# Performance work log

Measured on AMD Instinct MI355X. Metric: run time of the kernel, lower is better.

## Reference

```python
import jax, jax.numpy as jnp
import numpy as np

N = 4096      # nodes / sequence length
E = 131072    # edges (avg degree 32)
DIN = 512     # input feature dim
D = 256       # hidden_dim == output_dim (d_model)
H = 2         # nhead
DFF = 2048    # TransformerEncoderLayer default dim_feedforward
EPS = 1e-5


def setup_inputs() -> dict:
    key = jax.random.key(0)
    ks = jax.random.split(key, 16)
    s = lambda k, shape, scale: jax.random.normal(k, shape, jnp.float32) * scale
    return {
        "x": jax.random.normal(ks[0], (N, DIN), jnp.float32),
        "edge_index": jax.random.randint(ks[1], (2, E), 0, N),
        "edge_weight": jax.random.uniform(ks[2], (E,), jnp.float32),
        "W_gcn": s(ks[3], (DIN, D), 1.0 / np.sqrt(DIN)),
        "b_gcn": jnp.zeros((D,), jnp.float32),
        "in_proj_w": s(ks[4], (3 * D, D), 1.0 / np.sqrt(D)),
        "in_proj_b": jnp.zeros((3 * D,), jnp.float32),
        "out_proj_w": s(ks[5], (D, D), 1.0 / np.sqrt(D)),
        "out_proj_b": jnp.zeros((D,), jnp.float32),
        "lin1_w": s(ks[6], (DFF, D), 1.0 / np.sqrt(D)),
        "lin1_b": jnp.zeros((DFF,), jnp.float32),
        "lin2_w": s(ks[7], (D, DFF), 1.0 / np.sqrt(DFF)),
        "lin2_b": jnp.zeros((D,), jnp.float32),
        "ln1_g": jnp.ones((D,), jnp.float32),
        "ln1_b": jnp.zeros((D,), jnp.float32),
        "ln2_g": jnp.ones((D,), jnp.float32),
        "ln2_b": jnp.zeros((D,), jnp.float32),
    }


def _layernorm(x, g, b):
    mu = jnp.mean(x, axis=-1, keepdims=True)
    var = jnp.mean(jnp.square(x - mu), axis=-1, keepdims=True)
    return (x - mu) * jax.lax.rsqrt(var + EPS) * g + b


def _gcn_conv(x, edge_index, edge_weight, W, b):
    # PyG GCNConv: linear transform, add self-loops (weight 1), symmetric
    # degree normalization, scatter-add aggregation at target nodes.
    loops = jnp.arange(N)
    src = jnp.concatenate([edge_index[0], loops])
    dst = jnp.concatenate([edge_index[1], loops])
    w = jnp.concatenate([edge_weight, jnp.ones((N,), edge_weight.dtype)])
    deg = jax.ops.segment_sum(w, dst, num_segments=N)
    dinv = jnp.where(deg > 0, jax.lax.rsqrt(deg), 0.0)
    norm = dinv[src] * w * dinv[dst]                        # [E+N]
    xw = x @ W                                              # [N, D]
    out = jax.ops.segment_sum(norm[:, None] * xw[src], dst, num_segments=N)
    return out + b


def _mha(x, in_w, in_b, out_w, out_b):
    dh = D // H
    qkv = x @ in_w.T + in_b                                 # [N, 3D]
    q, k, v = jnp.split(qkv, 3, axis=-1)
    q = q.reshape(N, H, dh)
    k = k.reshape(N, H, dh)
    v = v.reshape(N, H, dh)
    scores = jnp.einsum("qhd,khd->hqk", q, k) / np.sqrt(dh)  # [H, N, N]
    attn = jax.nn.softmax(scores, axis=-1)
    o = jnp.einsum("hqk,khd->qhd", attn, v).reshape(N, D)
    return o @ out_w.T + out_b


def reference(x, edge_index, edge_weight, W_gcn, b_gcn, in_proj_w, in_proj_b,
              out_proj_w, out_proj_b, lin1_w, lin1_b, lin2_w, lin2_b,
              ln1_g, ln1_b, ln2_g, ln2_b):
    h = jax.nn.relu(_gcn_conv(x, edge_index, edge_weight, W_gcn, b_gcn))
    # TransformerEncoderLayer, post-norm (norm_first=False), dropout=eval
    h = _layernorm(h + _mha(h, in_proj_w, in_proj_b, out_proj_w, out_proj_b),
                   ln1_g, ln1_b)
    ff = jax.nn.relu(h @ lin1_w.T + lin1_b) @ lin2_w.T + lin2_b
    return _layernorm(h + ff, ln2_g, ln2_b)
```

## Files before the change

kernel.cpp:

```cpp
#include <hip/hip_runtime.h>
#include <hip/hip_bf16.h>

#define N_NODES 4096
#define E_EDGES 131072
#define DIN_    512
#define DM_     256
#define DFF_    2048
#define EPS_    1e-5f
#define NSPLIT  8

typedef __attribute__((ext_vector_type(8))) short bf16x8;
typedef __attribute__((ext_vector_type(4))) float f32x4;

__device__ __forceinline__ short f2b(float f) {
    union { float f; unsigned u; } x; x.f = f;
    unsigned r = x.u + 0x7fff + ((x.u >> 16) & 1);
    return (short)(r >> 16);
}

__device__ __forceinline__ void gload16(const void* g, void* l) {
    __builtin_amdgcn_global_load_lds(
        (const __attribute__((address_space(1))) void*)g,
        (__attribute__((address_space(3))) void*)l, 16, 0, 0);
}

__global__ __launch_bounds__(256)
void castall_kernel(const float* __restrict__ x, short* __restrict__ xb,
                    const float* __restrict__ inw, short* __restrict__ inwb,
                    const float* __restrict__ ow, short* __restrict__ owb,
                    const float* __restrict__ l1w, short* __restrict__ l1wb,
                    const float* __restrict__ l2w, short* __restrict__ l2wb,
                    const float* __restrict__ Wg, short* __restrict__ WgT) {
    const int b = blockIdx.x;
    __shared__ float t[32][33];
    if (b >= 3328) {
        const int b2 = b - 3328;
        const int bk = (b2 & 15) * 32, bn = (b2 >> 4) * 32;
        const int tx = threadIdx.x & 31, ty = threadIdx.x >> 5;
        #pragma unroll
        for (int i = 0; i < 4; ++i) {
            int r = ty + i * 8;
            t[r][tx] = Wg[(size_t)(bk + r) * DM_ + bn + tx];
        }
        __syncthreads();
        #pragma unroll
        for (int i = 0; i < 4; ++i) {
            int r = ty + i * 8;
            WgT[(size_t)(bn + r) * DIN_ + bk + tx] = f2b(t[tx][r]);
        }
        return;
    }
    const float* s; short* d; int base;
    if (b < 2048)      { s = x;   d = xb;   base = b * 256; }
    else if (b < 2240) { s = inw; d = inwb; base = (b - 2048) * 256; }
    else if (b < 2304) { s = ow;  d = owb;  base = (b - 2240) * 256; }
    else if (b < 2816) { s = l1w; d = l1wb; base = (b - 2304) * 256; }
    else               { s = l2w; d = l2wb; base = (b - 2816) * 256; }
    const int i = base + threadIdx.x;
    float4 v = reinterpret_cast<const float4*>(s)[i];
    union { short s[4]; int2 v; } o;
    o.s[0] = f2b(v.x); o.s[1] = f2b(v.y); o.s[2] = f2b(v.z); o.s[3] = f2b(v.w);
    reinterpret_cast<int2*>(d)[i] = o.v;
}

template<bool BF16OUT, bool RELU, bool SPLITK>
__global__ __launch_bounds__(256)
void mgemm_kernel(const short* __restrict__ A, const short* __restrict__ B,
                  const float* __restrict__ bias,
                  float* __restrict__ Cf, short* __restrict__ Cb,
                  short* __restrict__ VTout,
                  int M, int N, int K, int lda, int ldb, int ldc, int kchunk)
{
    __shared__ __align__(16) short As[128 * 32];
    __shared__ __align__(16) short Bs[128 * 32];
    const int tid = threadIdx.x;
    const int lane = tid & 63, w = tid >> 6;
    const int c = lane & 15, g = lane >> 4;
    const int wm = (w >> 1) * 64, wn = (w & 1) * 64;
    const int bm = blockIdx.y * 128, bn = blockIdx.x * 128;
    int k0 = 0, kend = K;
    if (SPLITK) { k0 = blockIdx.z * kchunk; kend = min(K, k0 + kchunk); }

    const int wbase = (tid & ~63) * 16;
    int srow[2], soff[2];
    #pragma unroll
    for (int i = 0; i < 2; ++i) {
        int L = i * 256 + tid;
        srow[i] = L >> 2;
        soff[i] = ((L & 3) ^ ((srow[i] >> 1) & 3)) * 8;
    }

    f32x4 acc[4][4] = {};
    for (int kb = k0; kb < kend; kb += 32) {
        #pragma unroll
        for (int i = 0; i < 2; ++i) {
            gload16(A + (size_t)(bm + srow[i]) * lda + kb + soff[i],
                    (char*)As + i * 4096 + wbase);
            gload16(B + (size_t)(bn + srow[i]) * ldb + kb + soff[i],
                    (char*)Bs + i * 4096 + wbase);
        }
        asm volatile("s_waitcnt vmcnt(0)" ::: "memory");
        __syncthreads();
        bf16x8 af[4], bf[4];
        #pragma unroll
        for (int mf = 0; mf < 4; ++mf) {
            int r = wm + mf * 16 + c;
            int sw = (g ^ ((r >> 1) & 3)) * 16;
            af[mf] = *reinterpret_cast<const bf16x8*>((const char*)As + r * 64 + sw);
        }
        #pragma unroll
        for (int nf = 0; nf < 4; ++nf) {
            int r = wn + nf * 16 + c;
            int sw = (g ^ ((r >> 1) & 3)) * 16;
            bf[nf] = *reinterpret_cast<const bf16x8*>((const char*)Bs + r * 64 + sw);
        }
        #pragma unroll
        for (int mf = 0; mf < 4; ++mf)
            #pragma unroll
            for (int nf = 0; nf < 4; ++nf)
                acc[mf][nf] = __builtin_amdgcn_mfma_f32_16x16x32_bf16(
                    af[mf], bf[nf], acc[mf][nf], 0, 0, 0);
        __syncthreads();
    }
    #pragma unroll
    for (int mf = 0; mf < 4; ++mf) {
        const int row = bm + wm + mf * 16 + g * 4;
        #pragma unroll
        for (int nf = 0; nf < 4; ++nf) {
            const int col = bn + wn + nf * 16 + c;
            float bv = bias ? bias[col] : 0.f;
            #pragma unroll
            for (int v = 0; v < 4; ++v) {
                float val = acc[mf][nf][v];
                size_t o = (size_t)(row + v) * ldc + col;
                if (SPLITK) {
                    if (blockIdx.z == 0) val += bv;
                    atomicAdd(&Cf[o], val);
                } else {
                    val += bv;
                    if (RELU) val = fmaxf(val, 0.f);
                    if (BF16OUT) {
                        short bvs = f2b(val);
                        Cb[o] = bvs;
                        if (VTout && col >= 512)
                            VTout[(size_t)(col - 512) * N_NODES + row + v] = bvs;
                    } else {
                        Cf[o] = val;
                    }
                }
            }
        }
    }
}

__global__ __launch_bounds__(256)
void fattn_kernel(const short* __restrict__ qkv, const short* __restrict__ VT,
                  short* __restrict__ Opart, float* __restrict__ ml)
{
    const int bid = blockIdx.x;
    const int j = bid >> 3;
    const int pair = 2 * (bid & 7) + (j & 1);
    const int hd = pair >> 3, sp = pair & 7;
    const int qt = j >> 1;
    const int tid = threadIdx.x;
    const int w = tid >> 6, lane = tid & 63;
    const int c = lane & 15, g = lane >> 4;
    const int q0 = qt * 64 + w * 16;

    __shared__ __align__(16) char smem[32768];
    char* KldsB = smem;
    char* VldsB = smem + 16384;
    short* Pw = (short*)(smem + w * 2816);

    const char* qkvC = (const char*)qkv;
    const char* vtC  = (const char*)VT;
    const int wbase = (tid & ~63) * 16;

    const short* Q = qkv + (size_t)q0 * 768 + hd * 128;
    bf16x8 qf[4];
    #pragma unroll
    for (int ks = 0; ks < 4; ++ks)
        qf[ks] = *reinterpret_cast<const bf16x8*>(Q + (size_t)c * 768 + ks * 32 + g * 8);

    auto stageKV = [&](int kt) {
        const int key0 = kt * 64;
        #pragma unroll
        for (int i = 0; i < 4; ++i) {
            int Lr  = i * 4096 + tid * 16;
            int key = Lr >> 8;
            int lg  = (Lr & 255) ^ ((key & 7) << 4);
            const char* src = qkvC + ((size_t)(key0 + key) * 768 + 256 + hd * 128) * 2 + lg;
            gload16(src, KldsB + i * 4096 + wbase);
        }
        #pragma unroll
        for (int i = 0; i < 4; ++i) {
            int Lr = i * 4096 + tid * 16;
            int dh = Lr >> 7;
            int lg = (Lr & 127) ^ ((dh & 7) << 4);
            const char* src = vtC + (size_t)(hd * 128 + dh) * 8192 + key0 * 2 + lg;
            gload16(src, VldsB + i * 4096 + wbase);
        }
    };

    f32x4 O[8] = {};
    float m[4]  = {-1e30f, -1e30f, -1e30f, -1e30f};
    float lsum[4] = {};
    const float C = 0.12751744f;

    stageKV(sp * 8);
    asm volatile("s_waitcnt vmcnt(0)" ::: "memory");
    __syncthreads();

    for (int t = 0; t < 8; ++t) {
        f32x4 S[4] = {};
        #pragma unroll
        for (int nf = 0; nf < 4; ++nf) {
            const int key = nf * 16 + c;
            const char* kr = KldsB + key * 256;
            const int sw = (key & 7) << 4;
            #pragma unroll
            for (int ks = 0; ks < 4; ++ks) {
                bf16x8 kf = *reinterpret_cast<const bf16x8*>(kr + ((ks * 64 + g * 16) ^ sw));
                S[nf] = __builtin_amdgcn_mfma_f32_16x16x32_bf16(qf[ks], kf, S[nf], 0, 0, 0);
            }
        }
        __syncthreads();

        float z[4][4];
        float lmax[4];
        bool ok = true;
        #pragma unroll
        for (int v = 0; v < 4; ++v) {
            #pragma unroll
            for (int nf = 0; nf < 4; ++nf) z[nf][v] = S[nf][v] * C;
            lmax[v] = fmaxf(fmaxf(z[0][v], z[1][v]), fmaxf(z[2][v], z[3][v]));
            ok = ok && (lmax[v] <= m[v] + 8.f);
        }
        if (!__all(ok)) {
            float mx[4];
            #pragma unroll
            for (int v = 0; v < 4; ++v) mx[v] = lmax[v];
            #pragma unroll
            for (int off = 1; off <= 8; off <<= 1)
                #pragma unroll
                for (int v = 0; v < 4; ++v) mx[v] = fmaxf(mx[v], __shfl_xor(mx[v], off));
            #pragma unroll
            for (int v = 0; v < 4; ++v) {
                float mn = fmaxf(m[v], mx[v]);
                float scl = exp2f(m[v] - mn);
                m[v] = mn;
                lsum[v] *= scl;
                #pragma unroll
                for (int nf2 = 0; nf2 < 8; ++nf2) O[nf2][v] *= scl;
            }
        }
        #pragma unroll
        for (int nf = 0; nf < 4; ++nf)
            #pragma unroll
            for (int v = 0; v < 4; ++v) {
                float p = exp2f(z[nf][v] - m[v]);
                lsum[v] += p;
                union { float f; unsigned u; } pu; pu.f = p;
                Pw[(4 * g + v) * 88 + nf * 16 + c] = (short)(pu.u >> 16);
            }
        bf16x8 pa[2];
        #pragma unroll
        for (int ks = 0; ks < 2; ++ks)
            pa[ks] = *reinterpret_cast<const bf16x8*>(Pw + c * 88 + ks * 32 + g * 8);
        #pragma unroll
        for (int nf2 = 0; nf2 < 8; ++nf2) {
            const int dh = nf2 * 16 + c;
            const char* vr = VldsB + dh * 128;
            const int sw = (dh & 7) << 4;
            #pragma unroll
            for (int ks = 0; ks < 2; ++ks) {
                bf16x8 vf = *reinterpret_cast<const bf16x8*>(vr + ((ks * 64 + g * 16) ^ sw));
                O[nf2] = __builtin_amdgcn_mfma_f32_16x16x32_bf16(pa[ks], vf, O[nf2], 0, 0, 0);
            }
        }
        __syncthreads();
        if (t < 7) {
            stageKV(sp * 8 + t + 1);
            asm volatile("s_waitcnt vmcnt(0)" ::: "memory");
            __syncthreads();
        }
    }
    #pragma unroll
    for (int off = 1; off <= 8; off <<= 1)
        #pragma unroll
        for (int v = 0; v < 4; ++v) lsum[v] += __shfl_xor(lsum[v], off);
    const size_t pbase = ((size_t)hd * NSPLIT + sp) * N_NODES;
    #pragma unroll
    for (int v = 0; v < 4; ++v) {
        const int row = q0 + 4 * g + v;
        const size_t rowo = (pbase + row) * 128;
        #pragma unroll
        for (int nf2 = 0; nf2 < 8; ++nf2)
            Opart[rowo + nf2 * 16 + c] = f2b(O[nf2][v]);
        if (c == 0) {
            ml[(pbase + row) * 2 + 0] = m[v];
            ml[(pbase + row) * 2 + 1] = lsum[v];
        }
    }
}

__global__ __launch_bounds__(256)
void attn_combine_kernel(const short* __restrict__ Opart, const float* __restrict__ ml,
                         short* __restrict__ attnb)
{
    const int row = blockIdx.x;
    const int hd = threadIdx.x >> 7, d = threadIdx.x & 127;
    float ms[NSPLIT], ls[NSPLIT];
    float mmax = -1e30f;
    #pragma unroll
    for (int s = 0; s < NSPLIT; ++s) {
        const size_t p = ((size_t)hd * NSPLIT + s) * N_NODES + row;
        ms[s] = ml[p * 2 + 0];
        ls[s] = ml[p * 2 + 1];
        mmax = fmaxf(mmax, ms[s]);
    }
    float lt = 0.f, acc = 0.f;
    #pragma unroll
    for (int s = 0; s < NSPLIT; ++s) {
        const float wgt = exp2f(ms[s] - mmax);
        lt += wgt * ls[s];
        const size_t p = ((size_t)hd * NSPLIT + s) * N_NODES + row;
        union { short s; unsigned short u; } b; b.s = Opart[p * 128 + d];
        union { unsigned u; float f; } cv; cv.u = ((unsigned)b.u) << 16;
        acc += wgt * cv.f;
    }
    attnb[(size_t)row * DM_ + hd * 128 + d] = f2b(acc / lt);
}

__global__ void deg_accum_kernel(const int* __restrict__ dst,
                                 const float* __restrict__ w,
                                 float* deg, int* count) {
    int e = blockIdx.x * 256 + threadIdx.x;
    if (e < E_EDGES) {
        int d = dst[e];
        atomicAdd(&deg[d], w[e]);
        atomicAdd(&count[d], 1);
    }
}
__global__ __launch_bounds__(256)
void csr_scan_kernel(const int* __restrict__ count, int* __restrict__ start,
                     int* __restrict__ cursor, float* __restrict__ deg) {
    __shared__ int sum[256];
    const int tid = threadIdx.x;
    const int base = tid * 16;
    #pragma unroll
    for (int i = 0; i < 16; ++i) {
        int n = base + i;
        deg[n] = rsqrtf(deg[n] + 1.0f);
    }
    int loc[16]; int s = 0;
    #pragma unroll
    for (int i = 0; i < 16; ++i) { loc[i] = count[base + i]; s += loc[i]; }
    sum[tid] = s;
    __syncthreads();
    for (int off = 1; off < 256; off <<= 1) {
        int v = (tid >= off) ? sum[tid - off] : 0;
        __syncthreads();
        sum[tid] += v;
        __syncthreads();
    }
    int run = sum[tid] - s;
    #pragma unroll
    for (int i = 0; i < 16; ++i) {
        start[base + i] = run;
        cursor[base + i] = run;
        run += loc[i];
    }
    if (tid == 255) start[N_NODES] = run;
}
__global__ void csr_fill_kernel(const int* __restrict__ src, const int* __restrict__ dst,
                                const float* __restrict__ w, const float* __restrict__ dinv,
                                int* __restrict__ cursor,
                                int* __restrict__ csr_src, float* __restrict__ csr_nrm) {
    int e = blockIdx.x * 256 + threadIdx.x;
    if (e >= E_EDGES) return;
    int s = src[e], d = dst[e];
    int pos = atomicAdd(&cursor[d], 1);
    csr_src[pos] = s;
    csr_nrm[pos] = dinv[s] * w[e] * dinv[d];
}
__global__ __launch_bounds__(256)
void gcn_gather_kernel(const int* __restrict__ start, const int* __restrict__ csr_src,
                       const float* __restrict__ csr_nrm, const float* __restrict__ xw,
                       const float* __restrict__ dinv, const float* __restrict__ b,
                       float* __restrict__ h, short* __restrict__ hb) {
    const int n = blockIdx.x, tid = threadIdx.x;
    const int q = tid >> 6, lane = tid & 63;
    const int s0 = start[n], s1 = start[n + 1];
    __shared__ int    ssrc[256];
    __shared__ float  snrm[256];
    __shared__ float4 red[4][64];
    float4 acc = {0.f, 0.f, 0.f, 0.f};
    for (int base = s0; base < s1; base += 256) {
        const int cnt = min(256, s1 - base);
        __syncthreads();
        if (tid < cnt) { ssrc[tid] = csr_src[base + tid]; snrm[tid] = csr_nrm[base + tid]; }
        __syncthreads();
        for (int j = q; j < cnt; j += 4) {
            const float4 xv = *reinterpret_cast<const float4*>(
                xw + (size_t)ssrc[j] * DM_ + lane * 4);
            const float wj = snrm[j];
            acc.x = fmaf(wj, xv.x, acc.x);
            acc.y = fmaf(wj, xv.y, acc.y);
            acc.z = fmaf(wj, xv.z, acc.z);
            acc.w = fmaf(wj, xv.w, acc.w);
        }
    }
    red[q][lane] = acc;
    __syncthreads();
    if (q == 0) {
        const float4 a1 = red[1][lane], a2 = red[2][lane], a3 = red[3][lane];
        const float di = dinv[n], d2 = di * di;
        const float4 xs = *reinterpret_cast<const float4*>(xw + (size_t)n * DM_ + lane * 4);
        const float4 bv = *reinterpret_cast<const float4*>(b + lane * 4);
        float v0 = fmaxf(acc.x + a1.x + a2.x + a3.x + d2 * xs.x + bv.x, 0.f);
        float v1 = fmaxf(acc.y + a1.y + a2.y + a3.y + d2 * xs.y + bv.y, 0.f);
        float v2 = fmaxf(acc.z + a1.z + a2.z + a3.z + d2 * xs.z + bv.z, 0.f);
        float v3 = fmaxf(acc.w + a1.w + a2.w + a3.w + d2 * xs.w + bv.w, 0.f);
        const size_t o = (size_t)n * DM_ + lane * 4;
        *reinterpret_cast<float4*>(h + o) = make_float4(v0, v1, v2, v3);
        union { short s[4]; int2 v; } ob;
        ob.s[0] = f2b(v0); ob.s[1] = f2b(v1); ob.s[2] = f2b(v2); ob.s[3] = f2b(v3);
        *reinterpret_cast<int2*>(hb + o) = ob.v;
    }
}

__global__ __launch_bounds__(256)
void ln_kernel(const float* __restrict__ a, const float* __restrict__ b,
               const float* __restrict__ g, const float* __restrict__ be,
               float* __restrict__ outf, short* __restrict__ outb,
               float* __restrict__ clearbuf) {
    const int n = blockIdx.x, d = threadIdx.x;
    const size_t idx = (size_t)n * DM_ + d;
    float x = a[idx] + b[idx];
    if (clearbuf) clearbuf[idx] = 0.f;
    float s = x;
    #pragma unroll
    for (int off = 32; off; off >>= 1) s += __shfl_xor(s, off);
    __shared__ float red[8];
    const int wid = d >> 6;
    if ((d & 63) == 0) red[wid] = s;
    __syncthreads();
    float mu = (red[0] + red[1] + red[2] + red[3]) * (1.f / 256.f);
    float c = x - mu;
    float q = c * c;
    #pragma unroll
    for (int off = 32; off; off >>= 1) q += __shfl_xor(q, off);
    if ((d & 63) == 0) red[4 + wid] = q;
    __syncthreads();
    float var = (red[4] + red[5] + red[6] + red[7]) * (1.f / 256.f);
    float v = c * rsqrtf(var + EPS_) * g[d] + be[d];
    outf[idx] = v;
    if (outb) outb[idx] = f2b(v);
}

extern "C" void kernel_launch(void* const* d_in, const int* in_sizes, int n_in,
                              void* d_out, int out_size, void* d_ws, size_t ws_size,
                              hipStream_t stream) {
    const float* x   = (const float*)d_in[0];
    const int*   ei  = (const int*)  d_in[1];
    const float* ew  = (const float*)d_in[2];
    const float* Wg  = (const float*)d_in[3];
    const float* bg  = (const float*)d_in[4];
    const float* inw = (const float*)d_in[5];
    const float* inb = (const float*)d_in[6];
    const float* ow  = (const float*)d_in[7];
    const float* ob  = (const float*)d_in[8];
    const float* l1w = (const float*)d_in[9];
    const float* l1b = (const float*)d_in[10];
    const float* l2w = (const float*)d_in[11];
    const float* l2b = (const float*)d_in[12];
    const float* g1  = (const float*)d_in[13];
    const float* b1  = (const float*)d_in[14];
    const float* g2  = (const float*)d_in[15];
    const float* b2  = (const float*)d_in[16];
    float* out = (float*)d_out;

    char* ws = (char*)d_ws;
    size_t off = 0;
    auto alloc = [&](size_t bytes) {
        void* p = ws + off;
        off += (bytes + 255) & ~(size_t)255;
        return p;
    };
    float* deg   = (float*)alloc((size_t)N_NODES * 4);
    int*   count = (int*)  alloc((size_t)N_NODES * 4);
    float* xw    = (float*)alloc((size_t)N_NODES * DM_ * 4);
    float* tmp   = (float*)alloc((size_t)N_NODES * DM_ * 4);
    size_t zspan = off;
    int*   startA  = (int*)  alloc((size_t)(N_NODES + 1) * 4);
    int*   cursor  = (int*)  alloc((size_t)N_NODES * 4);
    int*   csr_src = (int*)  alloc((size_t)E_EDGES * 4);
    float* csr_nrm = (float*)alloc((size_t)E_EDGES * 4);
    short* xb    = (short*)alloc((size_t)N_NODES * DIN_ * 2);
    short* WgT   = (short*)alloc((size_t)DM_ * DIN_ * 2);
    short* inwb  = (short*)alloc((size_t)768 * DM_ * 2);
    short* owb   = (short*)alloc((size_t)DM_ * DM_ * 2);
    short* l1wb  = (short*)alloc((size_t)DFF_ * DM_ * 2);
    short* l2wb  = (short*)alloc((size_t)DM_ * DFF_ * 2);
    float* h     = (float*)alloc((size_t)N_NODES * DM_ * 4);
    short* hb    = (short*)alloc((size_t)N_NODES * DM_ * 2);
    short* qkvb  = (short*)alloc((size_t)N_NODES * 768 * 2);
    short* VT    = (short*)alloc((size_t)DM_ * N_NODES * 2);
    short* attnb = (short*)alloc((size_t)N_NODES * DM_ * 2);
    float* h1    = (float*)alloc((size_t)N_NODES * DM_ * 4);
    short* h1b   = (short*)alloc((size_t)N_NODES * DM_ * 2);
    size_t opart_b = (size_t)2 * NSPLIT * N_NODES * 128 * 2;
    size_t ml_b    = (size_t)2 * NSPLIT * N_NODES * 2 * 4;
    size_t ff1_b   = (size_t)N_NODES * DFF_ * 2;
    char*  R     = (char*)alloc(opart_b + ml_b > ff1_b ? opart_b + ml_b : ff1_b);
    short* Opart = (short*)R;
    float* ml    = (float*)(R + opart_b);
    short* ff1b  = (short*)R;
    (void)ws_size; (void)in_sizes; (void)n_in; (void)out_size;

    const int* srcI = ei;
    const int* dstI = ei + E_EDGES;

    hipMemsetAsync(ws, 0, zspan, stream);
    castall_kernel<<<3456, 256, 0, stream>>>(x, xb, inw, inwb, ow, owb,
                                             l1w, l1wb, l2w, l2wb, Wg, WgT);

    deg_accum_kernel<<<E_EDGES / 256, 256, 0, stream>>>(dstI, ew, deg, count);
    csr_scan_kernel<<<1, 256, 0, stream>>>(count, startA, cursor, deg);
    csr_fill_kernel<<<E_EDGES / 256, 256, 0, stream>>>(srcI, dstI, ew, deg, cursor,
                                                       csr_src, csr_nrm);
    mgemm_kernel<false, false, true><<<dim3(2, 32, 4), 256, 0, stream>>>(
        xb, WgT, nullptr, xw, nullptr, nullptr,
        N_NODES, DM_, DIN_, DIN_, DIN_, DM_, 128);
    gcn_gather_kernel<<<N_NODES, 256, 0, stream>>>(startA, csr_src, csr_nrm, xw,
                                                   deg, bg, h, hb);

    mgemm_kernel<true, false, false><<<dim3(6, 32), 256, 0, stream>>>(
        hb, inwb, inb, nullptr, qkvb, VT,
        N_NODES, 768, DM_, DM_, DM_, 768, 0);

    fattn_kernel<<<1024, 256, 0, stream>>>(qkvb, VT, Opart, ml);
    attn_combine_kernel<<<N_NODES, 256, 0, stream>>>(Opart, ml, attnb);

    mgemm_kernel<false, false, true><<<dim3(2, 32, 2), 256, 0, stream>>>(
        attnb, owb, ob, tmp, nullptr, nullptr,
        N_NODES, DM_, DM_, DM_, DM_, DM_, 128);
    ln_kernel<<<N_NODES, 256, 0, stream>>>(h, tmp, g1, b1, h1, h1b, tmp);

    mgemm_kernel<true, true, false><<<dim3(16, 32), 256, 0, stream>>>(
        h1b, l1wb, l1b, nullptr, ff1b, nullptr,
        N_NODES, DFF_, DM_, DM_, DM_, DFF_, 0);
    mgemm_kernel<false, false, true><<<dim3(2, 32, 4), 256, 0, stream>>>(
        ff1b, l2wb, l2b, tmp, nullptr, nullptr,
        N_NODES, DM_, DFF_, DFF_, DFF_, DM_, 512);
    ln_kernel<<<N_NODES, 256, 0, stream>>>(h1, tmp, g2, b2, out, nullptr, nullptr);
}
```

Measured before the change: 203.5 us.

## Double-buffer GEMM LDS tiles and overlap K/V loads in flash attention

The bf16 GEMM now uses two LDS buffers and prefetches the next K-slice while computing on the current one, with partial vmcnt waits and raw barriers in place of full drains. The attention kernel splits K and V staging: the next K tile loads during softmax and the PV product, and the next V tile loads during the following QK product. The P scratch moves to its own LDS region so it no longer aliases the K buffer. This hides global-to-LDS latency behind MFMA work, at the cost of more LDS per block (which can lower occupancy) and correctness that depends on the vmcnt counting.

```diff
diff --git a/kernel.cpp b/kernel.cpp
--- a/kernel.cpp
+++ b/kernel.cpp
@@ -71,8 +71,8 @@
                   short* __restrict__ VTout,
                   int M, int N, int K, int lda, int ldb, int ldc, int kchunk)
 {
-    __shared__ __align__(16) short As[128 * 32];
-    __shared__ __align__(16) short Bs[128 * 32];
+    __shared__ __align__(16) short As[2][128 * 32];
+    __shared__ __align__(16) short Bs[2][128 * 32];
     const int tid = threadIdx.x;
     const int lane = tid & 63, w = tid >> 6;
     const int c = lane & 15, g = lane >> 4;
@@ -90,29 +90,38 @@
         soff[i] = ((L & 3) ^ ((srow[i] >> 1) & 3)) * 8;
     }
 
-    f32x4 acc[4][4] = {};
-    for (int kb = k0; kb < kend; kb += 32) {
+    auto stage = [&](int b, int kb) {
         #pragma unroll
         for (int i = 0; i < 2; ++i) {
             gload16(A + (size_t)(bm + srow[i]) * lda + kb + soff[i],
-                    (char*)As + i * 4096 + wbase);
+                    (char*)As[b] + i * 4096 + wbase);
             gload16(B + (size_t)(bn + srow[i]) * ldb + kb + soff[i],
-                    (char*)Bs + i * 4096 + wbase);
-        }
-        asm volatile("s_waitcnt vmcnt(0)" ::: "memory");
-        __syncthreads();
+                    (char*)Bs[b] + i * 4096 + wbase);
+        }
+    };
+
+    const int nsteps = (kend - k0) >> 5;
+    f32x4 acc[4][4] = {};
+    stage(0, k0);
+    for (int s = 0; s < nsteps; ++s) {
+        const int cur = s & 1;
+        const bool pf = (s + 1 < nsteps);
+        if (pf) stage(cur ^ 1, k0 + (s + 1) * 32);
+        if (pf) asm volatile("s_waitcnt vmcnt(4)" ::: "memory");
+        else    asm volatile("s_waitcnt vmcnt(0)" ::: "memory");
+        __builtin_amdgcn_s_barrier();
         bf16x8 af[4], bf[4];
         #pragma unroll
         for (int mf = 0; mf < 4; ++mf) {
             int r = wm + mf * 16 + c;
             int sw = (g ^ ((r >> 1) & 3)) * 16;
-            af[mf] = *reinterpret_cast<const bf16x8*>((const char*)As + r * 64 + sw);
+            af[mf] = *reinterpret_cast<const bf16x8*>((const char*)As[cur] + r * 64 + sw);
         }
         #pragma unroll
         for (int nf = 0; nf < 4; ++nf) {
             int r = wn + nf * 16 + c;
             int sw = (g ^ ((r >> 1) & 3)) * 16;
-            bf[nf] = *reinterpret_cast<const bf16x8*>((const char*)Bs + r * 64 + sw);
+            bf[nf] = *reinterpret_cast<const bf16x8*>((const char*)Bs[cur] + r * 64 + sw);
         }
         #pragma unroll
         for (int mf = 0; mf < 4; ++mf)
@@ -120,7 +129,7 @@
             for (int nf = 0; nf < 4; ++nf)
                 acc[mf][nf] = __builtin_amdgcn_mfma_f32_16x16x32_bf16(
                     af[mf], bf[nf], acc[mf][nf], 0, 0, 0);
-        __syncthreads();
+        __builtin_amdgcn_s_barrier();
     }
     #pragma unroll
     for (int mf = 0; mf < 4; ++mf) {
@@ -167,10 +176,10 @@
     const int c = lane & 15, g = lane >> 4;
     const int q0 = qt * 64 + w * 16;
 
-    __shared__ __align__(16) char smem[32768];
+    __shared__ __align__(16) char smem[44032];
     char* KldsB = smem;
     char* VldsB = smem + 16384;
-    short* Pw = (short*)(smem + w * 2816);
+    short* Pw = (short*)(smem + 32768 + w * 2816);
 
     const char* qkvC = (const char*)qkv;
     const char* vtC  = (const char*)VT;
@@ -182,7 +191,7 @@
     for (int ks = 0; ks < 4; ++ks)
         qf[ks] = *reinterpret_cast<const bf16x8*>(Q + (size_t)c * 768 + ks * 32 + g * 8);
 
-    auto stageKV = [&](int kt) {
+    auto stageK = [&](int kt) {
         const int key0 = kt * 64;
         #pragma unroll
         for (int i = 0; i < 4; ++i) {
@@ -192,6 +201,9 @@
             const char* src = qkvC + ((size_t)(key0 + key) * 768 + 256 + hd * 128) * 2 + lg;
             gload16(src, KldsB + i * 4096 + wbase);
         }
+    };
+    auto stageV = [&](int kt) {
+        const int key0 = kt * 64;
         #pragma unroll
         for (int i = 0; i < 4; ++i) {
             int Lr = i * 4096 + tid * 16;
@@ -207,11 +219,12 @@
     float lsum[4] = {};
     const float C = 0.12751744f;
 
-    stageKV(sp * 8);
-    asm volatile("s_waitcnt vmcnt(0)" ::: "memory");
-    __syncthreads();
+    stageK(sp * 8);
+    stageV(sp * 8);
 
     for (int t = 0; t < 8; ++t) {
+        asm volatile("s_waitcnt vmcnt(4)" ::: "memory");
+        __builtin_amdgcn_s_barrier();
         f32x4 S[4] = {};
         #pragma unroll
         for (int nf = 0; nf < 4; ++nf) {
@@ -224,7 +237,8 @@
                 S[nf] = __builtin_amdgcn_mfma_f32_16x16x32_bf16(qf[ks], kf, S[nf], 0, 0, 0);
             }
         }
-        __syncthreads();
+        __builtin_amdgcn_s_barrier();
+        if (t < 7) stageK(sp * 8 + t + 1);
 
         float z[4][4];
         float lmax[4];
@@ -263,6 +277,9 @@
                 union { float f; unsigned u; } pu; pu.f = p;
                 Pw[(4 * g + v) * 88 + nf * 16 + c] = (short)(pu.u >> 16);
             }
+        if (t < 7) asm volatile("s_waitcnt vmcnt(4)" ::: "memory");
+        else       asm volatile("s_waitcnt vmcnt(0)" ::: "memory");
+        __builtin_amdgcn_s_barrier();
         bf16x8 pa[2];
         #pragma unroll
         for (int ks = 0; ks < 2; ++ks)
@@ -278,12 +295,8 @@
                 O[nf2] = __builtin_amdgcn_mfma_f32_16x16x32_bf16(pa[ks], vf, O[nf2], 0, 0, 0);
             }
         }
-        __syncthreads();
-        if (t < 7) {
-            stageKV(sp * 8 + t + 1);
-            asm volatile("s_waitcnt vmcnt(0)" ::: "memory");
-            __syncthreads();
-        }
+        __builtin_amdgcn_s_barrier();
+        if (t < 7) stageV(sp * 8 + t + 1);
     }
     #pragma unroll
     for (int off = 1; off <= 8; off <<= 1)
```

Measured after the change: 194.5 us. 4.5% less time.
